# Kernel optimization log

Hardware: AMD Instinct MI355X
Metric: run time of the kernel (lower is better)

Reference implementation:

```python
import jax, jax.numpy as jnp
import numpy as np

N = 512   # particles
T = 128   # timesteps
V_L = 3.4
V_0 = 4.2
GAMMA = 0.9
ALPHA = 0.15
BETA = 15.0
E_CRIT_INV = 2e-5
F_STD = 0.05
G_STD = 0.02
NU = 1.0 / (G_STD * float(np.sqrt(2.0 * np.pi)))
CUR_MIN = 0.0
CUR_MAX = 1.0


def voc(soc):
    # open-circuit voltage model
    return (V_L + (V_0 - V_L) * jnp.exp(GAMMA * (soc - 1.0))
            + ALPHA * V_L * (soc - 1.0)
            + (1.0 - ALPHA) * V_L * (jnp.exp(-BETA) - jnp.exp(-BETA * jnp.sqrt(soc))))


def mlp(x, w1, b1, w2, b2, w3, b3):
    h = jax.nn.sigmoid(x @ w1 + b1)
    h = jax.nn.sigmoid(h @ w2 + b2)
    return h @ w3 + b3


def setup_inputs() -> dict:
    key = jax.random.key(0)
    ks = jax.random.split(key, 11)
    soc_init = jax.random.uniform(ks[0], (N, 1), jnp.float32, 0.6, 1.0)
    current = jax.random.uniform(ks[1], (1, T), jnp.float32)
    voltage_measured = 3.4 + 0.8 * jax.random.uniform(ks[2], (1, T), jnp.float32)
    noise = jax.random.normal(ks[3], (T, N, 1), jnp.float32)
    u = jax.random.uniform(ks[4], (T,), jnp.float32)
    w1 = jax.random.normal(ks[5], (2, 1024), jnp.float32) / np.float32(np.sqrt(2.0))
    b1 = jnp.zeros((1024,), jnp.float32)
    w2 = jax.random.normal(ks[6], (1024, 512), jnp.float32) / np.float32(np.sqrt(1024.0))
    b2 = jnp.zeros((512,), jnp.float32)
    w3 = jax.random.normal(ks[7], (512, 1), jnp.float32) / np.float32(np.sqrt(512.0))
    b3 = jnp.zeros((1,), jnp.float32)
    return {"soc_init": soc_init, "current": current, "voltage_measured": voltage_measured,
            "noise": noise, "u": u, "w1": w1, "b1": b1, "w2": w2, "b2": b2, "w3": w3, "b3": b3}


def reference(soc_init, current, voltage_measured, noise, u, w1, b1, w2, b2, w3, b3):
    n = soc_init.shape[0]
    # pre-loop step: V at t=0 conditions
    I0 = current[0, 0] * jnp.ones_like(soc_init)
    sI0 = (I0 - CUR_MIN) / (CUR_MAX - CUR_MIN)
    Z0 = mlp(jnp.concatenate([soc_init, sI0], axis=1), w1, b1, w2, b2, w3, b3)
    V0 = voc(soc_init) - I0 * Z0

    log_n = jnp.log(jnp.float32(n))

    def step(carry, xs):
        soc, I, V = carry
        cur_t, vmeas_t, noise_t, u_t = xs
        # state propagation with process noise, then clamp to (0, 1]
        soc = soc - I * V * E_CRIT_INV + F_STD * noise_t
        soc = jnp.where(soc > 1.0, 1.0, jnp.where(soc < 0.0, 1e-10, soc))
        I = cur_t * jnp.ones_like(soc)
        sI = (I - CUR_MIN) / (CUR_MAX - CUR_MIN)
        Z = mlp(jnp.concatenate([soc, sI], axis=1), w1, b1, w2, b2, w3, b3)  # [N,1]
        V = voc(soc) - I * Z                                                 # [N,1]
        # importance weights / step loss (logsumexp trick as in source)
        logW = jnp.log(jnp.float32(NU)) - 0.5 * jnp.square((V - vmeas_t) / G_STD)
        step_loss = jax.nn.logsumexp(logW) - log_n
        # systematic resampling on normalized weights
        wn = jax.nn.softmax(logW[:, 0])          # normalized weights [N]
        cum = jnp.cumsum(wn)
        pos = (jnp.arange(n, dtype=jnp.float32) + u_t) / jnp.float32(n)
        idx = jnp.clip(jnp.searchsorted(cum, pos), 0, n - 1)
        soc_r = soc[idx]
        return (soc_r, I, V), (V[:, 0], soc_r[:, 0], step_loss)

    xs = (current[0], voltage_measured[0], noise, u)
    _, (v_hist, s_hist, losses) = jax.lax.scan(step, (soc_init, I0, V0), xs)
    loss = jnp.sum(losses)
    voltage = v_hist.T    # [N, T]
    soc_hist = s_hist.T   # [N, T]
    return loss, voltage, soc_hist
```

## Files before the change

kernel.cpp:

```cpp
#include <hip/hip_runtime.h>
#include <math.h>

#define NP 512
#define TS 128
#define GI 33
#define TAB2D (GI * GI)
#define GV 193
#define V_Lc 3.4f
#define V_0c 4.2f
#define GAMMAc 0.9f
#define ALPHAc 0.15f
#define BETAc 15.0f
#define E_INV 2e-5f
#define F_STDc 0.05f
#define G_STDc 0.02f

#define LBAR() asm volatile("s_waitcnt lgkmcnt(0)\n\ts_barrier" ::: "memory")

__device__ __forceinline__ float sigmoid_jax(float x) {
    float e = expf(-fabsf(x));
    float num = (x >= 0.f) ? 1.f : e;
    return num / (1.f + e);
}

__device__ __forceinline__ float vocf(float s) {
    float sm1 = s - 1.f;
    return V_Lc + (V_0c - V_Lc) * expf(GAMMAc * sm1)
         + (ALPHAc * V_Lc) * sm1
         + (1.f - ALPHAc) * V_Lc * (expf(-BETAc) - expf(-BETAc * sqrtf(s)));
}

template <int R>
__device__ __forceinline__ int dpp_ror(int v) {
    return __builtin_amdgcn_update_dpp(0, v, 0x120 | R, 0xf, 0xf, false);
}
template <int S>
__device__ __forceinline__ int dpp_shr(int v) {
    return __builtin_amdgcn_update_dpp(0, v, 0x110 | S, 0xf, 0xf, true);
}
__device__ __forceinline__ float rdlane_f(float v, int l) {
    return __int_as_float(__builtin_amdgcn_readlane(__float_as_int(v), l));
}

__device__ __forceinline__ float wave_max_f(float v) {
    v = fmaxf(v, __int_as_float(dpp_ror<1>(__float_as_int(v))));
    v = fmaxf(v, __int_as_float(dpp_ror<2>(__float_as_int(v))));
    v = fmaxf(v, __int_as_float(dpp_ror<4>(__float_as_int(v))));
    v = fmaxf(v, __int_as_float(dpp_ror<8>(__float_as_int(v))));
    int iv = __float_as_int(v);
    v = fmaxf(v, __int_as_float(__builtin_amdgcn_update_dpp(iv, iv, 0x142, 0xf, 0xf, false)));
    iv = __float_as_int(v);
    v = fmaxf(v, __int_as_float(__builtin_amdgcn_update_dpp(iv, iv, 0x143, 0xf, 0xf, false)));
    return rdlane_f(v, 63);
}

__device__ __forceinline__ int wave_max_i(int v) {
    v = max(v, dpp_ror<1>(v));
    v = max(v, dpp_ror<2>(v));
    v = max(v, dpp_ror<4>(v));
    v = max(v, dpp_ror<8>(v));
    v = max(v, __builtin_amdgcn_update_dpp(v, v, 0x142, 0xf, 0xf, false));
    v = max(v, __builtin_amdgcn_update_dpp(v, v, 0x143, 0xf, 0xf, false));
    return __builtin_amdgcn_readlane(v, 63);
}

__device__ __forceinline__ float wave_scan_add(float v, int lane) {
    v += __int_as_float(dpp_shr<1>(__float_as_int(v)));
    v += __int_as_float(dpp_shr<2>(__float_as_int(v)));
    v += __int_as_float(dpp_shr<4>(__float_as_int(v)));
    v += __int_as_float(dpp_shr<8>(__float_as_int(v)));
    float s15 = rdlane_f(v, 15);
    float s31 = rdlane_f(v, 31);
    float s47 = rdlane_f(v, 47);
    int row = lane >> 4;
    if (row >= 1) v += s15;
    if (row >= 2) v += s31;
    if (row >= 3) v += s47;
    return v;
}

__device__ __forceinline__ int wave_scanmax_i(int v, int lane) {
    v = max(v, dpp_shr<1>(v));
    v = max(v, dpp_shr<2>(v));
    v = max(v, dpp_shr<4>(v));
    v = max(v, dpp_shr<8>(v));
    int r15 = __builtin_amdgcn_readlane(v, 15);
    int r31 = __builtin_amdgcn_readlane(v, 31);
    int r47 = __builtin_amdgcn_readlane(v, 47);
    int row = lane >> 4;
    if (row >= 1) v = max(v, r15);
    if (row >= 2) v = max(v, r31);
    if (row >= 3) v = max(v, r47);
    return v;
}

__device__ __forceinline__ float interp33(const float* __restrict__ row, float s) {
    float x = s * 32.0f;
    int j = (int)floorf(x);
    j = j < 0 ? 0 : (j > 31 ? 31 : j);
    int st = j - 1;
    st = st < 0 ? 0 : (st > 29 ? 29 : st);
    float uu = x - (float)st;
    float um0 = uu, um1 = uu - 1.f, um2 = uu - 2.f, um3 = uu - 3.f;
    float c0 = um1 * um2 * um3 * (-1.f / 6.f);
    float c1 = um0 * um2 * um3 * (0.5f);
    float c2 = um0 * um1 * um3 * (-0.5f);
    float c3 = um0 * um1 * um2 * (1.f / 6.f);
    return c0 * row[st] + c1 * row[st + 1] + c2 * row[st + 2] + c3 * row[st + 3];
}

__device__ __forceinline__ float interp193(const float* __restrict__ row, float s) {
    float x = s * 192.0f;
    int j = (int)floorf(x);
    j = j < 0 ? 0 : (j > 191 ? 191 : j);
    int st = j - 1;
    st = st < 0 ? 0 : (st > 189 ? 189 : st);
    float uu = x - (float)st;
    float um0 = uu, um1 = uu - 1.f, um2 = uu - 2.f, um3 = uu - 3.f;
    float c0 = um1 * um2 * um3 * (-1.f / 6.f);
    float c1 = um0 * um2 * um3 * (0.5f);
    float c2 = um0 * um1 * um3 * (-0.5f);
    float c3 = um0 * um1 * um2 * (1.f / 6.f);
    return c0 * row[st] + c1 * row[st + 1] + c2 * row[st + 2] + c3 * row[st + 3];
}

__device__ __forceinline__ int count_le(float C, float u) {
    int h = (int)floorf(C - u);
    h = h < -1 ? -1 : (h > 511 ? 511 : h);
    h += (int)((h < 511) && (((float)(h + 1) + u) <= C));
    h -= (int)((h >= 0) && (((float)h + u) > C));
    return h + 1;
}

#define BKT 32
__global__ __launch_bounds__(256) void k_tab(
    const float* __restrict__ w1, const float* __restrict__ b1,
    const float* __restrict__ w2, const float* __restrict__ b2,
    const float* __restrict__ w3, float* __restrict__ zpart)
{
    const int tid = threadIdx.x;
    const int rowblk = blockIdx.x >> 1;
    const int colhalf = blockIdx.x & 1;
    const int r0 = rowblk * 16;
    const int cbase = colhalf * 256;

    __shared__ float As[16][BKT + 1];
    __shared__ float Bs[BKT][256];
    __shared__ float srow[16], irow[16];

    if (tid < 16) {
        int r = r0 + tid;
        r = r > (TAB2D - 1) ? (TAB2D - 1) : r;
        int si = r / GI;
        int ii = r - si * GI;
        srow[tid] = (float)si * (1.0f / 32.0f);
        irow[tid] = (float)ii * (1.0f / 32.0f);
    }
    __syncthreads();

    const int rg = tid >> 5;
    const int ct = tid & 31;
    float acc[2][8];
    #pragma unroll
    for (int a = 0; a < 2; ++a)
        #pragma unroll
        for (int b = 0; b < 8; ++b) acc[a][b] = 0.f;

    for (int kk = 0; kk < 1024; kk += BKT) {
        #pragma unroll
        for (int h = 0; h < 2; ++h) {
            int idx = tid + h * 256;
            int row = idx >> 5, k = idx & 31, kc = kk + k;
            float pre = srow[row] * w1[kc] + irow[row] * w1[1024 + kc] + b1[kc];
            As[row][k] = sigmoid_jax(pre);
        }
        #pragma unroll
        for (int jj = 0; jj < 8; ++jj) {
            int vi = tid + jj * 256;
            int k = vi >> 6, c4 = vi & 63;
            *(float4*)&Bs[k][c4 * 4] = *(const float4*)&w2[(kk + k) * 512 + cbase + c4 * 4];
        }
        __syncthreads();
        #pragma unroll
        for (int k = 0; k < BKT; ++k) {
            float a0 = As[rg * 2][k];
            float a1 = As[rg * 2 + 1][k];
            float bq[8];
            *(float4*)&bq[0] = *(const float4*)&Bs[k][ct * 4];
            *(float4*)&bq[4] = *(const float4*)&Bs[k][ct * 4 + 128];
            #pragma unroll
            for (int q = 0; q < 8; ++q) {
                acc[0][q] += a0 * bq[q];
                acc[1][q] += a1 * bq[q];
            }
        }
        __syncthreads();
    }

    float b2r[8], w3r[8];
    *(float4*)&b2r[0] = *(const float4*)&b2[cbase + ct * 4];
    *(float4*)&b2r[4] = *(const float4*)&b2[cbase + ct * 4 + 128];
    *(float4*)&w3r[0] = *(const float4*)&w3[cbase + ct * 4];
    *(float4*)&w3r[4] = *(const float4*)&w3[cbase + ct * 4 + 128];
    #pragma unroll
    for (int rr = 0; rr < 2; ++rr) {
        float zp = 0.f;
        #pragma unroll
        for (int q = 0; q < 8; ++q)
            zp += w3r[q] * sigmoid_jax(acc[rr][q] + b2r[q]);
        #pragma unroll
        for (int mm = 1; mm < 32; mm <<= 1) zp += __shfl_xor(zp, mm);
        if (ct == 0 && (r0 + rg * 2 + rr) < TAB2D)
            zpart[colhalf * TAB2D + r0 + rg * 2 + rr] = zp;
    }
}

__global__ __launch_bounds__(512, 1) void k_seq(
    const float* __restrict__ zpart, const float* __restrict__ soc_init,
    const float* __restrict__ current, const float* __restrict__ vmeas,
    const float* __restrict__ u, const float* __restrict__ noise,
    const float* __restrict__ b3, float* __restrict__ out)
{
    const int tid = threadIdx.x;
    const int lane = tid & 63;
    const int wv = tid >> 6;

    __shared__ float vt[TS][GV];
    __shared__ float zt[TS][GI];
    __shared__ float zt2d[TAB2D];
    __shared__ float vocs[GV];
    __shared__ float socs[2][NP];
    __shared__ int marker[NP];
    __shared__ float cur_s[TS], vm_s[TS], u_s[TS];
    __shared__ float redM[8], redT[8];

    float bb3 = b3[0];
    for (int j = tid; j < TAB2D; j += 512) zt2d[j] = zpart[j] + zpart[TAB2D + j] + bb3;
    if (tid < TS) { cur_s[tid] = current[tid]; vm_s[tid] = vmeas[tid]; u_s[tid] = u[tid]; }
    if (tid < GV) vocs[tid] = vocf((float)tid * (1.0f / 192.0f));
    marker[tid] = 0;
    __syncthreads();
    for (int idx = tid; idx < TS * GI; idx += 512) {
        int t = idx / GI, g = idx - t * GI;
        zt[t][g] = interp33(&zt2d[g * GI], cur_s[t]);
    }
    __syncthreads();
    for (int idx = tid; idx < TS * GV; idx += 512) {
        int t = idx / GV, j = idx - t * GV;
        float sj = (float)j * (1.0f / 192.0f);
        vt[t][j] = vocs[j] - cur_s[t] * interp33(&zt[t][0], sj);
    }
    __syncthreads();

    float soc = soc_init[tid];
    float Iprev = cur_s[0];
    float V = interp193(&vt[0][0], soc);
    float loss_acc = 0.f;
    const float LOG_NU = logf(19.947114020071635f);
    const float LOG_N = logf(512.f);
    float nz_cur = noise[tid];
    float* outV = out + 1 + tid * TS;
    float* outS = out + 1 + NP * TS + tid * TS;

    for (int t = 0; t < TS; ++t) {
        int tn = (t + 1 < TS) ? t + 1 : t;
        float nz_next = noise[tn * 512 + tid];

        soc = soc - Iprev * V * E_INV + F_STDc * nz_cur;
        soc = soc > 1.f ? 1.f : (soc < 0.f ? 1e-10f : soc);
        socs[t & 1][tid] = soc;

        V = interp193(&vt[t][0], soc);
        float d = (V - vm_s[t]) * (1.f / G_STDc);
        float lw = LOG_NU - 0.5f * d * d;

        float m = wave_max_f(lw);
        float e = __expf(lw - m);
        float incl = wave_scan_add(e, lane);
        if (lane == 63) { redM[wv] = m; redT[wv] = incl; }
        LBAR();

        float rm = redM[lane & 7];
        float rt = redT[lane & 7];
        float M = rm;
        M = fmaxf(M, __int_as_float(dpp_ror<1>(__float_as_int(M))));
        M = fmaxf(M, __int_as_float(dpp_ror<2>(__float_as_int(M))));
        M = fmaxf(M, __int_as_float(dpp_ror<4>(__float_as_int(M))));
        M = fmaxf(M, __int_as_float(dpp_ror<8>(__float_as_int(M))));
        float fw = __expf(rm - M);
        float term = rt * fw;
        float sc = term;
        sc += __int_as_float(dpp_shr<1>(__float_as_int(sc)));
        sc += __int_as_float(dpp_shr<2>(__float_as_int(sc)));
        sc += __int_as_float(dpp_shr<4>(__float_as_int(sc)));
        float S = rdlane_f(sc, 7);
        float off = 0.f;
        if (wv > 0) off = rdlane_f(sc, wv - 1);
        float fw_own = rdlane_f(fw, wv);
        loss_acc += M + __logf(S) - LOG_N;

        float C = 512.f * ((off + incl * fw_own) / S);
        int hi = count_le(C, u_s[t]);
        if (hi < 512) atomicMax(&marker[hi], (t << 10) | (tid + 1));
        LBAR();

        int pm = 0;
        for (int w = 0; w < wv; ++w) pm = max(pm, marker[w * 64 + lane]);
        pm = wave_max_i(pm);
        int v = wave_scanmax_i(marker[tid], lane);
        int sv = max(v, pm);
        int owner = ((sv >> 10) == t) ? (sv & 1023) : 0;
        owner = owner > 511 ? 511 : owner;
        float socr = socs[t & 1][owner];

        outV[t] = V;
        outS[t] = socr;
        soc = socr;
        Iprev = cur_s[t];
        nz_cur = nz_next;
    }
    if (tid == 0) out[0] = loss_acc;
}

extern "C" void kernel_launch(void* const* d_in, const int* in_sizes, int n_in,
                              void* d_out, int out_size, void* d_ws, size_t ws_size,
                              hipStream_t stream)
{
    const float* soc_init = (const float*)d_in[0];
    const float* current  = (const float*)d_in[1];
    const float* vmeas    = (const float*)d_in[2];
    const float* noise    = (const float*)d_in[3];
    const float* u        = (const float*)d_in[4];
    const float* w1 = (const float*)d_in[5];
    const float* b1 = (const float*)d_in[6];
    const float* w2 = (const float*)d_in[7];
    const float* b2 = (const float*)d_in[8];
    const float* w3 = (const float*)d_in[9];
    const float* b3 = (const float*)d_in[10];
    float* out = (float*)d_out;
    float* ws  = (float*)d_ws;

    float* zpart = ws;

    k_tab<<<138, 256, 0, stream>>>(w1, b1, w2, b2, w3, zpart);
    k_seq<<<1, 512, 0, stream>>>(zpart, soc_init, current, vmeas, u, noise, b3, out);
}
```

Measured before the change: 285.1 us.

## Stage outputs time-major in workspace and transpose in separate kernel

The sequential kernel now writes V and resampled soc to time-major workspace buffers with coalesced per-step stores, instead of strided per-particle rows. A new tiled transpose kernel then writes them out in [N,T] layout. The per-wave max and sum are also packed into one float2 shared load, and a redundant DPP max step is removed. This adds an extra kernel launch and a round trip of the output through global memory.

```diff
diff --git a/kernel.cpp b/kernel.cpp
--- a/kernel.cpp
+++ b/kernel.cpp
@@ -219,7 +219,8 @@
     const float* __restrict__ zpart, const float* __restrict__ soc_init,
     const float* __restrict__ current, const float* __restrict__ vmeas,
     const float* __restrict__ u, const float* __restrict__ noise,
-    const float* __restrict__ b3, float* __restrict__ out)
+    const float* __restrict__ b3, float* __restrict__ vbuf,
+    float* __restrict__ sbuf, float* __restrict__ out)
 {
     const int tid = threadIdx.x;
     const int lane = tid & 63;
@@ -232,7 +233,7 @@
     __shared__ float socs[2][NP];
     __shared__ int marker[NP];
     __shared__ float cur_s[TS], vm_s[TS], u_s[TS];
-    __shared__ float redM[8], redT[8];
+    __shared__ float2 redMT[8];
 
     float bb3 = b3[0];
     for (int j = tid; j < TAB2D; j += 512) zt2d[j] = zpart[j] + zpart[TAB2D + j] + bb3;
@@ -259,8 +260,6 @@
     const float LOG_NU = logf(19.947114020071635f);
     const float LOG_N = logf(512.f);
     float nz_cur = noise[tid];
-    float* outV = out + 1 + tid * TS;
-    float* outS = out + 1 + NP * TS + tid * TS;
 
     for (int t = 0; t < TS; ++t) {
         int tn = (t + 1 < TS) ? t + 1 : t;
@@ -271,22 +270,23 @@
         socs[t & 1][tid] = soc;
 
         V = interp193(&vt[t][0], soc);
+        vbuf[t * 512 + tid] = V;
         float d = (V - vm_s[t]) * (1.f / G_STDc);
         float lw = LOG_NU - 0.5f * d * d;
 
         float m = wave_max_f(lw);
         float e = __expf(lw - m);
         float incl = wave_scan_add(e, lane);
-        if (lane == 63) { redM[wv] = m; redT[wv] = incl; }
+        if (lane == 63) redMT[wv] = make_float2(m, incl);
         LBAR();
 
-        float rm = redM[lane & 7];
-        float rt = redT[lane & 7];
+        float2 rmt = redMT[lane & 7];
+        float rm = rmt.x;
+        float rt = rmt.y;
         float M = rm;
         M = fmaxf(M, __int_as_float(dpp_ror<1>(__float_as_int(M))));
         M = fmaxf(M, __int_as_float(dpp_ror<2>(__float_as_int(M))));
         M = fmaxf(M, __int_as_float(dpp_ror<4>(__float_as_int(M))));
-        M = fmaxf(M, __int_as_float(dpp_ror<8>(__float_as_int(M))));
         float fw = __expf(rm - M);
         float term = rt * fw;
         float sc = term;
@@ -313,13 +313,32 @@
         owner = owner > 511 ? 511 : owner;
         float socr = socs[t & 1][owner];
 
-        outV[t] = V;
-        outS[t] = socr;
+        sbuf[t * 512 + tid] = socr;
         soc = socr;
         Iprev = cur_s[t];
         nz_cur = nz_next;
     }
     if (tid == 0) out[0] = loss_acc;
+}
+
+__global__ __launch_bounds__(256) void k_fin(
+    const float* __restrict__ vbuf, const float* __restrict__ sbuf,
+    float* __restrict__ out)
+{
+    __shared__ float tile[32][33];
+    int tz = blockIdx.z;
+    int t0 = blockIdx.x * 32;
+    int i0 = blockIdx.y * 32;
+    const float* src = tz ? sbuf : vbuf;
+    float* dst = out + 1 + tz * (NP * TS);
+    int tx = threadIdx.x & 31, ty = threadIdx.x >> 5;
+    #pragma unroll
+    for (int m2 = 0; m2 < 4; ++m2)
+        tile[ty + 8 * m2][tx] = src[(t0 + ty + 8 * m2) * 512 + i0 + tx];
+    __syncthreads();
+    #pragma unroll
+    for (int m2 = 0; m2 < 4; ++m2)
+        dst[(i0 + ty + 8 * m2) * 128 + t0 + tx] = tile[tx][ty + 8 * m2];
 }
 
 extern "C" void kernel_launch(void* const* d_in, const int* in_sizes, int n_in,
@@ -341,7 +360,11 @@
     float* ws  = (float*)d_ws;
 
     float* zpart = ws;
+    float* vbuf  = ws + 2180;
+    float* sbuf  = vbuf + NP * TS;
 
     k_tab<<<138, 256, 0, stream>>>(w1, b1, w2, b2, w3, zpart);
-    k_seq<<<1, 512, 0, stream>>>(zpart, soc_init, current, vmeas, u, noise, b3, out);
-}
+    k_seq<<<1, 512, 0, stream>>>(zpart, soc_init, current, vmeas, u, noise, b3,
+                                 vbuf, sbuf, out);
+    k_fin<<<dim3(4, 16, 2), 256, 0, stream>>>(vbuf, sbuf, out);
+}
```

Result: faster. 259.6 us (-8.9%).
